# Optimization experiments

Measured on AMD Instinct MI355X. Metric: run time of the kernel, lower is better.

## Reference

```python
import jax, jax.numpy as jnp
import numpy as np

N, T, D, H = 256, 512, 256, 256


def setup_inputs() -> dict:
    key = jax.random.key(0)
    ks = jax.random.split(key, 9)
    scale_x = float(np.sqrt(6.0 / (D + H)))  # xavier_uniform range approx
    scale_h = float(np.sqrt(6.0 / (H + H)))
    def wx(k):
        return jax.random.uniform(k, (D, H), jnp.float32, -scale_x, scale_x)
    def wh(k):
        return jax.random.uniform(k, (H, H), jnp.float32, -scale_h, scale_h)
    inp = {
        'x': jax.random.normal(ks[0], (N, T, D), jnp.float32),
        'w_ii': wx(ks[1]), 'w_hi': wh(ks[2]),
        'w_if': wx(ks[3]), 'w_hf': wh(ks[4]),
        'w_ig': wx(ks[5]), 'w_hg': wh(ks[6]),
        'w_io': wx(ks[7]), 'w_ho': wh(ks[8]),
        # init_hidden() zeros all 1-D params
        'b_ii': jnp.zeros((H,), jnp.float32), 'b_hi': jnp.zeros((H,), jnp.float32),
        'b_if': jnp.zeros((H,), jnp.float32), 'b_hf': jnp.zeros((H,), jnp.float32),
        'b_ig': jnp.zeros((H,), jnp.float32), 'b_hg': jnp.zeros((H,), jnp.float32),
        'b_io': jnp.zeros((H,), jnp.float32), 'b_ho': jnp.zeros((H,), jnp.float32),
    }
    return inp


def reference(x, w_ii, w_hi, w_if, w_hf, w_ig, w_hg, w_io, w_ho,
              b_ii, b_hi, b_if, b_hf, b_ig, b_hg, b_io, b_ho):
    # Fuse the 4 input projections and 4 hidden projections into 2 GEMMs
    # (mathematically identical to the 8 separate matmuls).
    Wx = jnp.concatenate([w_ii, w_if, w_ig, w_io], axis=1)  # (D, 4H)
    Wh = jnp.concatenate([w_hi, w_hf, w_hg, w_ho], axis=1)  # (H, 4H)
    b = jnp.concatenate([b_ii + b_hi, b_if + b_hf, b_ig + b_hg, b_io + b_ho])  # (4H,)
    n, t, _ = x.shape
    h = x.shape[2]  # noqa (not used)
    # Precompute input projections for all timesteps: (T, N, 4H)
    xW = jnp.einsum('ntd,dg->tng', x, Wx)
    h0 = jnp.zeros((n, w_hi.shape[0]), x.dtype)
    c0 = jnp.zeros_like(h0)

    def step(carry, xw_t):
        h_t, c_t = carry
        gates = xw_t + h_t @ Wh + b  # (N, 4H)
        i_t, f_t, g_t, o_t = jnp.split(gates, 4, axis=1)
        i_t = jax.nn.sigmoid(i_t)
        f_t = jax.nn.sigmoid(f_t)
        g_t = jnp.tanh(g_t)
        o_t = jax.nn.sigmoid(o_t)
        c_t = f_t * c_t + i_t * g_t
        h_t = o_t * jnp.tanh(c_t)
        return (h_t, c_t), None

    (h_T, c_T), _ = jax.lax.scan(step, (h0, c0), xW)
    return (h_T, c_T)
```

## Files before the change

### kernel.cpp

```cpp
#include <hip/hip_runtime.h>
#include <cstdint>

typedef float  f32x4  __attribute__((ext_vector_type(4)));
typedef __bf16 bf16x8 __attribute__((ext_vector_type(8)));
typedef int    i32x4  __attribute__((ext_vector_type(4)));
typedef unsigned short u16;
typedef u16 u16x4 __attribute__((ext_vector_type(4)));

#define TT 512

__device__ __forceinline__ u16 f2bf(float f) {
  unsigned u = __builtin_bit_cast(unsigned, f);
  unsigned r = u + 0x7fffu + ((u >> 16) & 1u);
  return (u16)(r >> 16);
}
__device__ __forceinline__ float bflo(unsigned d) { return __builtin_bit_cast(float, d << 16); }
__device__ __forceinline__ float bfhi(unsigned d) { return __builtin_bit_cast(float, d & 0xffff0000u); }
__device__ __forceinline__ float rcpf(float x) { return __builtin_amdgcn_rcpf(x); }
__device__ __forceinline__ float fsig(float x) { return rcpf(1.f + __expf(-x)); }
__device__ __forceinline__ float ftanh(float x) { return 1.f - 2.f * rcpf(1.f + __expf(2.f * x)); }
__device__ __forceinline__ void gload_lds16(const u16* g, u16* l) {
  __builtin_amdgcn_global_load_lds((const __attribute__((address_space(1))) void*)(g),
                                   (__attribute__((address_space(3))) void*)(l), 16, 0, 0);
}

__global__ __launch_bounds__(256) void prep_w(
    const float* __restrict__ wii, const float* __restrict__ whi,
    const float* __restrict__ wif, const float* __restrict__ whf,
    const float* __restrict__ wig, const float* __restrict__ whg,
    const float* __restrict__ wio, const float* __restrict__ who,
    const float* __restrict__ bii, const float* __restrict__ bhi,
    const float* __restrict__ bif, const float* __restrict__ bhf,
    const float* __restrict__ big_, const float* __restrict__ bhg,
    const float* __restrict__ bio, const float* __restrict__ bho,
    u16* __restrict__ Wxb, signed char* __restrict__ Whq,
    float* __restrict__ wscale, float* __restrict__ bsum) {
  __shared__ float red[256];
  int b = blockIdx.x;
  int tid = threadIdx.x;
  if (b < 1024) {
    const float* wx[4] = {wii, wif, wig, wio};
    int G = b >> 8, h = b & 255;
    Wxb[b * 256 + tid] = f2bf(wx[G][tid * 256 + h]);
  } else if (b < 2048) {
    const float* wh[4] = {whi, whf, whg, who};
    int cidx = b - 1024;
    int G = cidx >> 8, h = cidx & 255;
    float w = wh[G][tid * 256 + h];
    red[tid] = fabsf(w);
    __syncthreads();
    for (int s = 128; s > 0; s >>= 1) {
      if (tid < s) red[tid] = fmaxf(red[tid], red[tid + s]);
      __syncthreads();
    }
    float mx = red[0];
    float scale = (mx > 0.f) ? mx * (1.f / 127.f) : 1.f;
    float qf = rintf(w / scale);
    qf = fminf(127.f, fmaxf(-127.f, qf));
    Whq[cidx * 256 + tid] = (signed char)(int)qf;
    if (tid == 0) wscale[cidx] = scale * (1.f / 127.f);
  } else {
    const float* bx[4] = {bii, bif, big_, bio};
    const float* bh[4] = {bhi, bhf, bhg, bho};
    for (int G = 0; G < 4; ++G) bsum[G * 256 + tid] = bx[G][tid] + bh[G][tid];
  }
}

__global__ __launch_bounds__(512, 2) void lstm_fused(
    const float* __restrict__ X, const u16* __restrict__ Bt,
    const float* __restrict__ bias, const signed char* __restrict__ Whq,
    const float* __restrict__ wscale, u16* __restrict__ xWp,
    int* __restrict__ rprog, float* __restrict__ out) {
  __shared__ u16 As[128 * 256];
  __shared__ u16 Bs[2][128 * 32];
  __shared__ __align__(16) signed char hb[2][576];
  int p = blockIdx.x;
  int tid = threadIdx.x;

  if (p >= 128) {
    int k = p - 128;
    int l = tid & 63, w8 = tid >> 6;
    int wm = w8 >> 2, wn = w8 & 3;
    int c = l & 15, q = l >> 4;
    int sw = (c & 7) << 4;
    int rowbase[4];
#pragma unroll
    for (int mt = 0; mt < 4; ++mt) rowbase[mt] = (wm * 64 + mt * 16 + c) * 512;

    for (int j = 0; j < 8; ++j) {
      int bm = j * 128 + k;
      {
        int trow = tid >> 2, ch = tid & 3;
        gload_lds16(Bt + (size_t)trow * 256 + ch * 8, &Bs[0][0] + tid * 8);
      }
#pragma unroll 4
      for (int jj = 0; jj < 16; ++jj) {
        int row_l = jj * 8 + w8;
        int d = l * 4;
        int r = bm * 128 + row_l;
        int t = r >> 8, n = r & 255;
        const float4 v = *(const float4*)(X + ((size_t)n * 512 + t) * 256 + d);
        u16x4 pk;
        pk[0] = f2bf(v.x); pk[1] = f2bf(v.y); pk[2] = f2bf(v.z); pk[3] = f2bf(v.w);
        int ba = (row_l * 512 + l * 8) ^ ((row_l & 7) << 4);
        *(u16x4*)((char*)As + ba) = pk;
      }
      __syncthreads();

      f32x4 acc[4][2];
#pragma unroll
      for (int i = 0; i < 4; ++i)
#pragma unroll
        for (int jn = 0; jn < 2; ++jn) acc[i][jn] = (f32x4){0.f, 0.f, 0.f, 0.f};

      for (int bn = 0; bn < 8; ++bn) {
#pragma unroll
        for (int ko = 0; ko < 8; ++ko) {
          int sn = bn * 8 + ko + 1;
          if (sn < 64) {
            int bnn = sn >> 3, kon = sn & 7;
            const u16* Bb = Bt + (size_t)(bnn * 128) * 256 + kon * 32;
            int trow = tid >> 2, ch = tid & 3;
            gload_lds16(Bb + (size_t)trow * 256 + ch * 8, &Bs[(ko + 1) & 1][0] + tid * 8);
          }
          bf16x8 af[4], bfr[2];
          const u16* bp = &Bs[ko & 1][0];
          int koff = (ko * 64 + q * 16) ^ sw;
#pragma unroll
          for (int mt = 0; mt < 4; ++mt)
            af[mt] = *(const bf16x8*)((const char*)As + rowbase[mt] + koff);
#pragma unroll
          for (int nt = 0; nt < 2; ++nt)
            bfr[nt] = *(const bf16x8*)(bp + (wn * 32 + nt * 16 + c) * 32 + q * 8);
#pragma unroll
          for (int mt = 0; mt < 4; ++mt)
#pragma unroll
            for (int nt = 0; nt < 2; ++nt)
              acc[mt][nt] = __builtin_amdgcn_mfma_f32_16x16x32_bf16(af[mt], bfr[nt], acc[mt][nt], 0, 0, 0);
          __syncthreads();
        }
#pragma unroll
        for (int mt = 0; mt < 4; ++mt) {
          int tm = bm * 8 + wm * 4 + mt;
#pragma unroll
          for (int nt = 0; nt < 2; ++nt) {
            int tn = bn * 8 + wn * 2 + nt;
            float bv = bias[tn * 16 + c];
            u16x4 pk;
#pragma unroll
            for (int r = 0; r < 4; ++r) pk[r] = f2bf(acc[mt][nt][r] + bv);
            *reinterpret_cast<u16x4*>(xWp + ((size_t)(tm * 64 + tn) * 256 + l * 4)) = pk;
            acc[mt][nt] = (f32x4){0.f, 0.f, 0.f, 0.f};
          }
        }
      }
      __syncthreads();
      if (tid == 0)
        __hip_atomic_fetch_add(&rprog[j], 1, __ATOMIC_RELEASE, __HIP_MEMORY_SCOPE_AGENT);
    }
    return;
  }

  int xcd = p & 7, q8 = (p >> 3) & 7, tsel = p >> 6;
  int G = xcd * 2 + tsel;
  int wid = tid >> 6, l = tid & 63;
  int c = l & 15, q = (l >> 4) & 3;
  int tt = q >> 1, rsel = q & 1;

  for (int i = tid; i < 288; i += 512) ((int*)hb)[i] = 0;

  i32x4 bw[4][2][4];
#pragma unroll
  for (int g = 0; g < 4; ++g)
#pragma unroll
    for (int ttl = 0; ttl < 2; ++ttl) {
      int col = g * 256 + wid * 32 + ttl * 16 + c;
#pragma unroll
      for (int ks = 0; ks < 4; ++ks)
        bw[g][ttl][ks] = *reinterpret_cast<const i32x4*>(Whq + (size_t)col * 256 + ks * 64 + q * 16);
    }
  float sc8[4];
#pragma unroll
  for (int g = 0; g < 4; ++g) sc8[g] = wscale[g * 256 + wid * 32 + tt * 16 + c];

  const char* xbase = (const char*)xWp + (size_t)G * 32768;
  int xoff[4];
#pragma unroll
  for (int g = 0; g < 4; ++g) {
    int tn = g * 16 + wid * 2 + tt;
    xoff[g] = tn * 512 + (((q8 >> 1) * 16 + c) * 8) + (q8 & 1) * 4;
  }

  if (tid == 0) {
    while (__hip_atomic_load(&rprog[0], __ATOMIC_RELAXED, __HIP_MEMORY_SCOPE_AGENT) < 128)
      __builtin_amdgcn_s_sleep(8);
    (void)__hip_atomic_load(&rprog[0], __ATOMIC_ACQUIRE, __HIP_MEMORY_SCOPE_AGENT);
  }
  __syncthreads();

  unsigned xw0[4], xw1[4];
#pragma unroll
  for (int g = 0; g < 4; ++g) xw0[g] = *(const unsigned*)(xbase + xoff[g]);
  xbase += 524288;

  i32x4 zacc = (i32x4){0, 0, 0, 0};
  float cs = 0.f, hh = 0.f;
  __syncthreads();

#define STEP(CUR, XW_CUR, XW_NXT)                                               \
  {                                                                             \
    _Pragma("unroll")                                                           \
    for (int g = 0; g < 4; ++g) XW_NXT[g] = *(const unsigned*)(xbase + xoff[g]);\
    const signed char* hr = hb[CUR ^ 1];                                        \
    i32x4 acc[4][2];                                                            \
    {                                                                           \
      i32x4 a0 = *(const i32x4*)(hr + (c & 1) * 288 + q * 16);                  \
      _Pragma("unroll")                                                         \
      for (int g = 0; g < 4; ++g) {                                             \
        __asm__("v_mfma_i32_16x16x64_i8 %0, %1, %2, %3"                         \
                : "=&v"(acc[g][0]) : "v"(a0), "a"(bw[g][0][0]), "v"(zacc));     \
        __asm__("v_mfma_i32_16x16x64_i8 %0, %1, %2, %3"                         \
                : "=&v"(acc[g][1]) : "v"(a0), "a"(bw[g][1][0]), "v"(zacc));     \
      }                                                                         \
    }                                                                           \
    _Pragma("unroll")                                                           \
    for (int ks = 1; ks < 4; ++ks) {                                            \
      i32x4 a = *(const i32x4*)(hr + (c & 1) * 288 + ks * 64 + q * 16);         \
      _Pragma("unroll")                                                         \
      for (int g = 0; g < 4; ++g) {                                             \
        __asm__("v_mfma_i32_16x16x64_i8 %0, %1, %2, %0"                         \
                : "+v"(acc[g][0]) : "v"(a), "a"(bw[g][0][ks]));                 \
        __asm__("v_mfma_i32_16x16x64_i8 %0, %1, %2, %0"                         \
                : "+v"(acc[g][1]) : "v"(a), "a"(bw[g][1][ks]));                 \
      }                                                                         \
    }                                                                           \
    __asm__ volatile("s_nop 7\n\ts_nop 7\n\ts_nop 7");   \
    float a4[4];                                                                \
    _Pragma("unroll")                                                           \
    for (int g = 0; g < 4; ++g) {                                               \
      int e = tt ? (rsel ? acc[g][1][1] : acc[g][1][0])                         \
                 : (rsel ? acc[g][0][1] : acc[g][0][0]);                        \
      unsigned d = XW_CUR[g];                                                   \
      float xv = rsel ? bfhi(d) : bflo(d);                                      \
      a4[g] = (float)e * sc8[g] + xv;                                           \
    }                                                                           \
    float gi = fsig(a4[0]);                                                     \
    float gf = fsig(a4[1]);                                                     \
    float gg = ftanh(a4[2]);                                                    \
    float go = fsig(a4[3]);                                                     \
    cs = gf * cs + gi * gg;                                                     \
    hh = go * ftanh(cs);                                                        \
    int hq = (int)rintf(hh * 127.f);                                            \
    hb[CUR][rsel * 288 + wid * 32 + tt * 16 + c] = (signed char)hq;             \
    xbase += 524288;                                                            \
    __builtin_amdgcn_s_waitcnt(0xC07F);   \
    __builtin_amdgcn_s_barrier();                                               \
  }

  for (int t = 0; t < TT; t += 2) {
    STEP(0, xw0, xw1)
    if (((t + 2) & 63) == 0 && (t + 2) < TT) {
      int j = (t + 2) >> 6;
      if (tid == 0) {
        while (__hip_atomic_load(&rprog[j], __ATOMIC_RELAXED, __HIP_MEMORY_SCOPE_AGENT) < 128)
          __builtin_amdgcn_s_sleep(8);
        (void)__hip_atomic_load(&rprog[j], __ATOMIC_ACQUIRE, __HIP_MEMORY_SCOPE_AGENT);
      }
      __syncthreads();
    }
    STEP(1, xw1, xw0)
  }
#undef STEP

  {
    int n = G * 16 + q8 * 2 + rsel;
    int hu = wid * 32 + tt * 16 + c;
    out[(size_t)n * 256 + hu] = hh;
    out[65536 + (size_t)n * 256 + hu] = cs;
  }
}

extern "C" void kernel_launch(void* const* d_in, const int* in_sizes, int n_in,
                              void* d_out, int out_size, void* d_ws, size_t ws_size,
                              hipStream_t stream) {
  const float* x   = (const float*)d_in[0];
  const float* wii = (const float*)d_in[1];
  const float* whi = (const float*)d_in[2];
  const float* wif = (const float*)d_in[3];
  const float* whf = (const float*)d_in[4];
  const float* wig = (const float*)d_in[5];
  const float* whg = (const float*)d_in[6];
  const float* wio = (const float*)d_in[7];
  const float* who = (const float*)d_in[8];
  const float* bii = (const float*)d_in[9];
  const float* bhi = (const float*)d_in[10];
  const float* bif = (const float*)d_in[11];
  const float* bhf = (const float*)d_in[12];
  const float* big_ = (const float*)d_in[13];
  const float* bhg = (const float*)d_in[14];
  const float* bio = (const float*)d_in[15];
  const float* bho = (const float*)d_in[16];

  char* ws = (char*)d_ws;
  int*   rprog  = (int*)(ws);
  u16*   Wxb    = (u16*)(ws + 67108864);
  signed char* Whq = (signed char*)(ws + 67633152);
  float* wscale = (float*)(ws + 67895296);
  float* bsum   = (float*)(ws + 67899392);
  u16*   xWp    = (u16*)(ws + 67903488);
  float* out = (float*)d_out;

  hipMemsetAsync(rprog, 0, 64, stream);
  prep_w<<<2049, 256, 0, stream>>>(wii, whi, wif, whf, wig, whg, wio, who,
                                   bii, bhi, bif, bhf, big_, bhg, bio, bho,
                                   Wxb, Whq, wscale, bsum);
  lstm_fused<<<256, 512, 0, stream>>>(x, Wxb, bsum, Whq, wscale, xWp, rprog, out);
}
```

Baseline: 637.7 us.

## Stage full 128x256 B panel in LDS per N-block instead of double-buffered K slices

The xW GEMM producer blocks now load a whole 128-column by 256-K slab of the weight matrix into LDS at once, using an XOR swizzle, rather than double-buffering 32-wide K slices. This removes the per-ko barrier and the fine-grained prefetch. The cost is a larger LDS footprint (an extra 64KB), which may lower occupancy. Load latency is also exposed between N-blocks, since each staging step is bracketed by barriers with no overlap.

After: 614.9 us. 3.6% less time.

```diff
diff --git a/kernel.cpp b/kernel.cpp
--- a/kernel.cpp
+++ b/kernel.cpp
@@ -72,7 +72,7 @@
     const float* __restrict__ wscale, u16* __restrict__ xWp,
     int* __restrict__ rprog, float* __restrict__ out) {
   __shared__ u16 As[128 * 256];
-  __shared__ u16 Bs[2][128 * 32];
+  __shared__ u16 Bp[128 * 256];
   __shared__ __align__(16) signed char hb[2][576];
   int p = blockIdx.x;
   int tid = threadIdx.x;
@@ -87,12 +87,22 @@
 #pragma unroll
     for (int mt = 0; mt < 4; ++mt) rowbase[mt] = (wm * 64 + mt * 16 + c) * 512;
 
+#define STAGE_B(BN)                                                             \
+    {                                                                           \
+      _Pragma("unroll")                                                         \
+      for (int s = 0; s < 8; ++s) {                                             \
+        int i = s * 512 + tid;                                                  \
+        int cl = i >> 5, wk = i & 31;                                           \
+        gload_lds16(Bt + (size_t)((BN) * 128 + cl) * 256 +                      \
+                        ((wk * 8) ^ ((cl & 7) << 3)),                           \
+                    Bp + i * 8);                                                \
+      }                                                                         \
+    }
+
     for (int j = 0; j < 8; ++j) {
       int bm = j * 128 + k;
-      {
-        int trow = tid >> 2, ch = tid & 3;
-        gload_lds16(Bt + (size_t)trow * 256 + ch * 8, &Bs[0][0] + tid * 8);
-      }
+      __syncthreads();
+      STAGE_B(0)
 #pragma unroll 4
       for (int jj = 0; jj < 16; ++jj) {
         int row_l = jj * 8 + w8;
@@ -116,28 +126,19 @@
       for (int bn = 0; bn < 8; ++bn) {
 #pragma unroll
         for (int ko = 0; ko < 8; ++ko) {
-          int sn = bn * 8 + ko + 1;
-          if (sn < 64) {
-            int bnn = sn >> 3, kon = sn & 7;
-            const u16* Bb = Bt + (size_t)(bnn * 128) * 256 + kon * 32;
-            int trow = tid >> 2, ch = tid & 3;
-            gload_lds16(Bb + (size_t)trow * 256 + ch * 8, &Bs[(ko + 1) & 1][0] + tid * 8);
-          }
           bf16x8 af[4], bfr[2];
-          const u16* bp = &Bs[ko & 1][0];
           int koff = (ko * 64 + q * 16) ^ sw;
 #pragma unroll
           for (int mt = 0; mt < 4; ++mt)
             af[mt] = *(const bf16x8*)((const char*)As + rowbase[mt] + koff);
 #pragma unroll
           for (int nt = 0; nt < 2; ++nt)
-            bfr[nt] = *(const bf16x8*)(bp + (wn * 32 + nt * 16 + c) * 32 + q * 8);
+            bfr[nt] = *(const bf16x8*)((const char*)Bp + (size_t)(wn * 32 + nt * 16 + c) * 512 + koff);
 #pragma unroll
           for (int mt = 0; mt < 4; ++mt)
 #pragma unroll
             for (int nt = 0; nt < 2; ++nt)
               acc[mt][nt] = __builtin_amdgcn_mfma_f32_16x16x32_bf16(af[mt], bfr[nt], acc[mt][nt], 0, 0, 0);
-          __syncthreads();
         }
 #pragma unroll
         for (int mt = 0; mt < 4; ++mt) {
@@ -153,11 +154,17 @@
             acc[mt][nt] = (f32x4){0.f, 0.f, 0.f, 0.f};
           }
         }
+        if (bn < 7) {
+          __syncthreads();
+          STAGE_B(bn + 1)
+          __syncthreads();
+        }
       }
       __syncthreads();
       if (tid == 0)
         __hip_atomic_fetch_add(&rprog[j], 1, __ATOMIC_RELEASE, __HIP_MEMORY_SCOPE_AGENT);
     }
+#undef STAGE_B
     return;
   }
 
```
